# Kernel tuning notes

Hardware: AMD Instinct MI355X
Metric: run time of the kernel (lower is better)

Reference implementation:

```python
import jax, jax.numpy as jnp
import numpy as np

C = 2048  # per-input channels; concat channels = 2*C = 4096
B, H, W = 2, 64, 64


def setup_inputs() -> dict:
    key = jax.random.key(0)
    ks = jax.random.split(key, 8)
    s = 0.02
    return {
        "f_rgb": jax.random.normal(ks[0], (B, C, H, W), jnp.float32),
        "f_i": jax.random.normal(ks[1], (B, C, H, W), jnp.float32),
        "wq": jax.random.normal(ks[2], (C, 2 * C), jnp.float32) * s,
        "bq": jnp.zeros((C,), jnp.float32),
        "wk": jax.random.normal(ks[3], (C, 2 * C), jnp.float32) * s,
        "bk": jnp.zeros((C,), jnp.float32),
        "wv": jax.random.normal(ks[4], (2 * C, 2 * C), jnp.float32) * s,
        "bv": jnp.zeros((2 * C,), jnp.float32),
    }


def reference(f_rgb, f_i, wq, bq, wk, bk, wv, bv):
    b, c, h, w = f_rgb.shape
    n = h * w
    # concat along channels: [B, 2C, N]
    x = jnp.concatenate([f_rgb, f_i], axis=1).reshape(b, 2 * c, n)
    # 1x1 convs == per-pixel matmuls over channels
    Q = jnp.einsum('oc,bcn->bon', wq, x) + bq[None, :, None]  # [B, C, N]
    K = jnp.einsum('oc,bcn->bon', wk, x) + bk[None, :, None]  # [B, C, N]
    V = jnp.einsum('oc,bcn->bon', wv, x) + bv[None, :, None]  # [B, 2C, N]
    scale = jnp.sqrt(jnp.asarray(2 * c, jnp.float32))  # sqrt(channels of concat)
    attn = jax.nn.softmax(jnp.einsum('bcn,bcm->bnm', Q, K) / scale, axis=-1)  # [B, N, N]
    # out[b,c,n] = sum_m V[b,c,m] * attn[b,n,m]  (bmm(V, attn^T))
    out = jnp.einsum('bcm,bnm->bcn', V, attn).reshape(b, 2 * c, h, w)
    f_final = out[:, :c] + out[:, c:]
    return (f_final, f_rgb, f_i, attn)
```

## Files before the change

### kernel.cpp

```cpp
#include <hip/hip_runtime.h>
#include <hip/hip_bf16.h>


#define B_   2
#define C_   2048
#define N_   4096
#define C2_  4096

#define LDSB 131072

typedef __hip_bfloat16 bf16_t;
typedef __bf16 bf16x8 __attribute__((ext_vector_type(8)));
typedef float floatx4 __attribute__((ext_vector_type(4)));

__device__ inline void load_lds16(const void* g, void* l) {
  __builtin_amdgcn_global_load_lds(
      (const __attribute__((address_space(1))) void*)g,
      (__attribute__((address_space(3))) void*)l, 16, 0, 0);
}

__device__ inline unsigned short f2bf(float f) {
  return __builtin_bit_cast(unsigned short, __float2bfloat16(f));
}

__device__ inline void cstore(float* p, float v)  { *p = v; }
__device__ inline void cstore(bf16_t* p, float v) { *p = __float2bfloat16(v); }

template <typename OutT>
__global__ __launch_bounds__(512, 2) void gemm_bt8(
    const bf16_t* __restrict__ A, const bf16_t* __restrict__ Bt,
    OutT* __restrict__ Cm, int K, int lda, int ldb, int ldc,
    long long abst, long long bbst, long long cbst,
    const float* __restrict__ bias_m, const float* __restrict__ bias_n,
    float scale)
{
  extern __shared__ char smem[];

  const int tid  = threadIdx.x;
  const int lane = tid & 63;
  const int wave = tid >> 6;
  const int wm   = wave >> 2;
  const int wn   = wave & 3;
  const int fr   = lane & 15;
  const int kc   = lane >> 4;

  const long long bM = (long long)blockIdx.y * 256;
  const long long bN = (long long)blockIdx.x * 256;

  const bf16_t* Ab = A  + (long long)blockIdx.z * abst;
  const bf16_t* Bb = Bt + (long long)blockIdx.z * bbst;
  OutT*         Cb = Cm + (long long)blockIdx.z * cbst;

  const int srow = lane >> 3;
  const int scol = 8 * ((lane & 7) ^ srow);
  const bf16_t* gA = Ab + (bM + wave * 8 + srow) * (long long)lda + scol;
  const bf16_t* gB = Bb + (bN + wave * 8 + srow) * (long long)ldb + scol;
  char* sbase = smem + wave * 1024;

  auto stage = [&](int p, int ab, int h, int kt) {
    const long long ld = ab ? ldb : lda;
    const bf16_t* g = (ab ? gB : gA) + (long long)h * 128 * ld
                                     + (long long)kt * 64;
    char* l = sbase + p * 65536 + ab * 32768 + h * 16384;
    load_lds16(g,            l);
    load_lds16(g + 64 * ld,  l + 8192);
  };

  floatx4 acc[8][4];
#pragma unroll
  for (int i = 0; i < 8; i++)
#pragma unroll
    for (int j = 0; j < 4; j++) acc[i][j] = (floatx4){0.f, 0.f, 0.f, 0.f};

  bf16x8 af[4][2];
  bf16x8 bfr[4][2];

  auto readAh = [&](int p, int mh) {
#pragma unroll
    for (int i = 0; i < 4; i++) {
      const int row = (mh * 4 + i) * 32 + wm * 16 + fr;
      const char* rb = smem + p * 65536 + row * 128;
#pragma unroll
      for (int ks = 0; ks < 2; ks++)
        af[i][ks] = *(const bf16x8*)(rb +
            (((ks * 64) + kc * 16) ^ ((fr & 7) << 4)));
    }
  };
  auto readBh = [&](int p, int nh) {
#pragma unroll
    for (int j = 0; j < 2; j++) {
      const int row = (nh * 2 + j) * 64 + wn * 16 + fr;
      const char* rb = smem + p * 65536 + 32768 + row * 128;
#pragma unroll
      for (int ks = 0; ks < 2; ks++)
        bfr[nh * 2 + j][ks] = *(const bf16x8*)(rb +
            (((ks * 64) + kc * 16) ^ ((fr & 7) << 4)));
    }
  };
  auto quad = [&](int mh, int nh) {
    __builtin_amdgcn_s_setprio(1);
#pragma unroll
    for (int i = 0; i < 4; i++)
#pragma unroll
      for (int j = 0; j < 2; j++)
#pragma unroll
        for (int ks = 0; ks < 2; ks++)
          acc[mh * 4 + i][nh * 2 + j] = __builtin_amdgcn_mfma_f32_16x16x32_bf16(
              af[i][ks], bfr[nh * 2 + j][ks], acc[mh * 4 + i][nh * 2 + j],
              0, 0, 0);
    __builtin_amdgcn_s_setprio(0);
  };

  const int NT = K >> 6;

  {
    const int t1 = (NT > 1) ? 1 : 0;
    stage(0, 0, 0, 0); stage(0, 1, 0, 0);
    stage(0, 0, 1, 0); stage(0, 1, 1, 0);
    stage(1, 0, 0, t1); stage(1, 1, 0, t1);
  }
  asm volatile("s_waitcnt vmcnt(4)" ::: "memory");
  __builtin_amdgcn_s_barrier();

  for (int t = 0; t < NT; ++t) {
    const int p  = t & 1, q = p ^ 1;
    const int t1 = (t + 1 < NT) ? t + 1 : NT - 1;
    const int t2 = (t + 2 < NT) ? t + 2 : NT - 1;

    readAh(p, 0); readBh(p, 0);
    stage(q, 0, 1, t1);
    __builtin_amdgcn_s_barrier();
    quad(0, 0);
    __builtin_amdgcn_s_barrier();

    readBh(p, 1);
    stage(q, 1, 1, t1);
    __builtin_amdgcn_s_barrier();
    quad(0, 1);
    __builtin_amdgcn_s_barrier();

    readAh(p, 1);
    stage(p, 0, 0, t2);
    __builtin_amdgcn_s_barrier();
    quad(1, 1);
    __builtin_amdgcn_s_barrier();

    stage(p, 1, 0, t2);
    __builtin_amdgcn_s_barrier();
    quad(1, 0);
    asm volatile("s_waitcnt vmcnt(4)" ::: "memory");
    __builtin_amdgcn_s_barrier();
  }

  const int rown = (lane >> 4) * 4;
#pragma unroll
  for (int mi = 0; mi < 8; mi++) {
#pragma unroll
    for (int ni = 0; ni < 4; ni++) {
      const long long n = bN + ni * 64 + wn * 16 + fr;
      const float bnv = bias_n ? bias_n[n] : 0.f;
#pragma unroll
      for (int r = 0; r < 4; r++) {
        const long long m = bM + mi * 32 + wm * 16 + rown + r;
        const float bmv = bias_m ? bias_m[m] : 0.f;
        cstore(&Cb[m * (long long)ldc + n], acc[mi][ni][r] * scale + bnv + bmv);
      }
    }
  }
}

__global__ __launch_bounds__(256) void pack_xt(
    const float* __restrict__ f_rgb, const float* __restrict__ f_i,
    float* __restrict__ out_rgb, float* __restrict__ out_i,
    bf16_t* __restrict__ xt)
{
  const int b  = blockIdx.z >> 1;
  const int wh = blockIdx.z & 1;
  const float* src = (wh ? f_i : f_rgb) + (long long)b * C_ * N_;
  float*       pt  = (wh ? out_i : out_rgb) + (long long)b * C_ * N_;
  const int c0 = blockIdx.y * 64, n0 = blockIdx.x * 64;
  __shared__ float tile[64][65];

  const int tid = threadIdx.x;
  {
    const int tn = tid & 63, tc4 = tid >> 6;
#pragma unroll
    for (int r = 0; r < 16; r++) {
      const int c = tc4 * 16 + r;
      const long long idx = (long long)(c0 + c) * N_ + n0 + tn;
      const float v = src[idx];
      pt[idx] = v;
      tile[tn][c] = v;
    }
  }
  __syncthreads();
  {
    const int tc = tid & 63, tn4 = tid >> 6;
#pragma unroll
    for (int r = 0; r < 16; r++) {
      const int n = tn4 * 16 + r;
      xt[((long long)b * N_ + n0 + n) * C2_ + wh * C_ + c0 + tc] =
          __float2bfloat16(tile[n][tc]);
    }
  }
}

__global__ __launch_bounds__(256) void conv_wqk(
    const float* __restrict__ wq, const float* __restrict__ wk,
    unsigned short* __restrict__ dst)
{
  const long long i = ((long long)blockIdx.x * 256 + threadIdx.x) * 4;
  const int o = (int)(i >> 12);
  const long long c = i & 4095;
  const float* src = (o < C_) ? (wq + (long long)o * C2_ + c)
                              : (wk + (long long)(o - C_) * C2_ + c);
  const float4 f = *(const float4*)src;
  *(ushort4*)(dst + i) = make_ushort4(f2bf(f.x), f2bf(f.y), f2bf(f.z), f2bf(f.w));
}

__global__ __launch_bounds__(256) void conv_wvsum(
    const float* __restrict__ wv, unsigned short* __restrict__ dst)
{
  const long long i = ((long long)blockIdx.x * 256 + threadIdx.x) * 4;
  const float4 a = *(const float4*)(wv + i);
  const float4 b = *(const float4*)(wv + i + (long long)C_ * C2_);
  *(ushort4*)(dst + i) = make_ushort4(f2bf(a.x + b.x), f2bf(a.y + b.y),
                                      f2bf(a.z + b.z), f2bf(a.w + b.w));
}

__global__ __launch_bounds__(256) void conv_bias(
    const float* __restrict__ bq, const float* __restrict__ bk,
    const float* __restrict__ bv, float* __restrict__ bqk,
    float* __restrict__ bvsum)
{
  const int i = blockIdx.x * 256 + threadIdx.x;
  bqk[i] = (i < C_) ? bq[i] : bk[i - C_];
  if (i < C_) bvsum[i] = bv[i] + bv[i + C_];
}

__global__ __launch_bounds__(256) void softmax_rows(
    float* __restrict__ attn, bf16_t* __restrict__ attn_bf)
{
  const long long row = blockIdx.x;
  float*  p  = attn    + row * N_;
  bf16_t* pb = attn_bf + row * N_;
  const int tid = threadIdx.x;
  const int lane = tid & 63, wave = tid >> 6;

  float v[16];
  float mx = -3.4e38f;
#pragma unroll
  for (int i = 0; i < 16; i++) { v[i] = p[tid + i * 256]; mx = fmaxf(mx, v[i]); }
#pragma unroll
  for (int off = 32; off >= 1; off >>= 1) mx = fmaxf(mx, __shfl_xor(mx, off, 64));

  __shared__ float redm[4];
  __shared__ float reds[4];
  if (lane == 0) redm[wave] = mx;
  __syncthreads();
  mx = fmaxf(fmaxf(redm[0], redm[1]), fmaxf(redm[2], redm[3]));

  float s = 0.f;
#pragma unroll
  for (int i = 0; i < 16; i++) { v[i] = __expf(v[i] - mx); s += v[i]; }
#pragma unroll
  for (int off = 32; off >= 1; off >>= 1) s += __shfl_xor(s, off, 64);
  if (lane == 0) reds[wave] = s;
  __syncthreads();
  s = reds[0] + reds[1] + reds[2] + reds[3];
  const float inv = 1.f / s;
#pragma unroll
  for (int i = 0; i < 16; i++) {
    const float a = v[i] * inv;
    p[tid + i * 256]  = a;
    pb[tid + i * 256] = __float2bfloat16(a);
  }
}

extern "C" void kernel_launch(void* const* d_in, const int* in_sizes, int n_in,
                              void* d_out, int out_size, void* d_ws, size_t ws_size,
                              hipStream_t stream) {
  const float* f_rgb = (const float*)d_in[0];
  const float* f_i   = (const float*)d_in[1];
  const float* wq    = (const float*)d_in[2];
  const float* bq    = (const float*)d_in[3];
  const float* wk    = (const float*)d_in[4];
  const float* bk    = (const float*)d_in[5];
  const float* wv    = (const float*)d_in[6];
  const float* bv    = (const float*)d_in[7];

  float* out       = (float*)d_out;
  float* out_ff    = out;
  float* out_rgb   = out + (size_t)B_ * C_ * N_;
  float* out_fi    = out_rgb + (size_t)B_ * C_ * N_;
  float* out_attn  = out_fi + (size_t)B_ * C_ * N_;

  char* ws = (char*)d_ws;
  size_t off = 0;
  auto alloc = [&](size_t bytes) {
    size_t o = off; off += (bytes + 255) & ~(size_t)255; return o;
  };
  bf16_t* xt   = (bf16_t*)(ws + alloc((size_t)B_ * N_ * C2_ * 2));
  bf16_t* wqk  = (bf16_t*)(ws + alloc((size_t)C2_ * C2_ * 2));
  bf16_t* wvs  = (bf16_t*)(ws + alloc((size_t)C_ * C2_ * 2));
  bf16_t* qkt  = (bf16_t*)(ws + alloc((size_t)B_ * N_ * C2_ * 2));
  bf16_t* vsum = (bf16_t*)(ws + alloc((size_t)B_ * C_ * N_ * 2));
  bf16_t* abf  = (bf16_t*)(ws + alloc((size_t)B_ * N_ * N_ * 2));
  float*  bqk  = (float*)(ws + alloc((size_t)C2_ * 4));
  float*  bvs  = (float*)(ws + alloc((size_t)C_ * 4));
  (void)ws_size; (void)in_sizes; (void)n_in; (void)out_size;

  static bool attr_done = false;
  if (!attr_done) {
    (void)hipFuncSetAttribute((const void*)&gemm_bt8<bf16_t>,
        hipFuncAttributeMaxDynamicSharedMemorySize, LDSB);
    (void)hipFuncSetAttribute((const void*)&gemm_bt8<float>,
        hipFuncAttributeMaxDynamicSharedMemorySize, LDSB);
    attr_done = true;
  }

  const dim3 blk(256);
  const dim3 blk8(512);

  pack_xt<<<dim3(N_ / 64, C_ / 64, B_ * 2), blk, 0, stream>>>(
      f_rgb, f_i, out_rgb, out_fi, xt);
  conv_wqk<<<dim3((C2_ * C2_) / (4 * 256)), blk, 0, stream>>>(
      wq, wk, (unsigned short*)wqk);
  conv_wvsum<<<dim3((C_ * C2_) / (4 * 256)), blk, 0, stream>>>(
      wv, (unsigned short*)wvs);
  conv_bias<<<dim3(C2_ / 256), blk, 0, stream>>>(bq, bk, bv, bqk, bvs);

  const long long sNN = (long long)N_ * C2_;
  const long long sCN = (long long)C_ * N_;

  gemm_bt8<bf16_t><<<dim3(C2_ / 256, N_ / 256, B_), blk8, LDSB, stream>>>(
      xt, wqk, qkt, C2_, C2_, C2_, C2_, sNN, 0, sNN, nullptr, bqk, 1.0f);

  gemm_bt8<bf16_t><<<dim3(N_ / 256, C_ / 256, B_), blk8, LDSB, stream>>>(
      wvs, xt, vsum, C2_, C2_, C2_, N_, 0, sNN, sCN, bvs, nullptr, 1.0f);

  gemm_bt8<float><<<dim3(N_ / 256, N_ / 256, B_), blk8, LDSB, stream>>>(
      qkt, qkt + C_, out_attn, C_, C2_, C2_, N_, sNN, sNN, sNN,
      nullptr, nullptr, 1.0f / 64.0f);

  softmax_rows<<<dim3(B_ * N_), blk, 0, stream>>>(out_attn, abf);

  gemm_bt8<float><<<dim3(N_ / 256, C_ / 256, B_), blk8, LDSB, stream>>>(
      vsum, abf, out_ff, N_, N_, N_, N_, sCN, sNN, sCN,
      nullptr, nullptr, 1.0f);
}
```

Baseline: 1.131 ms.

## Swizzle GEMM workgroup order, deepen LDS prefetch, reorder MFMA loop, vectorize softmax

The GEMM kernel remaps linear workgroup IDs round-robin across eight groups, likely to spread consecutive tiles across the XCDs for better L2 locality. It also issues one more half-tile load ahead in the prologue and shifts the staging schedule so the global-to-LDS prefetch runs deeper, with the vmcnt wait raised to match. The MFMA loop is reordered so the k-step is outermost. Separately, the softmax kernel now uses float4 and ushort4 vector loads and stores in place of scalar accesses. The remapping assumes the workgroup count is divisible by eight, and the new staging order must keep buffer reuse hazards correct.

```diff
diff --git a/kernel.cpp b/kernel.cpp
--- a/kernel.cpp
+++ b/kernel.cpp
@@ -44,12 +44,22 @@
   const int fr   = lane & 15;
   const int kc   = lane >> 4;
 
-  const long long bM = (long long)blockIdx.y * 256;
-  const long long bN = (long long)blockIdx.x * 256;
-
-  const bf16_t* Ab = A  + (long long)blockIdx.z * abst;
-  const bf16_t* Bb = Bt + (long long)blockIdx.z * bbst;
-  OutT*         Cb = Cm + (long long)blockIdx.z * cbst;
+  const int gx  = gridDim.x, gy = gridDim.y;
+  const int nxy = gx * gy;
+  const int nwg = nxy * gridDim.z;
+  int wg = blockIdx.x + gx * (blockIdx.y + gy * blockIdx.z);
+  wg = (wg & 7) * (nwg >> 3) + (wg >> 3);
+  const int bz  = wg / nxy;
+  const int rxy = wg - bz * nxy;
+  const int by  = rxy / gx;
+  const int bx  = rxy - by * gx;
+
+  const long long bM = (long long)by * 256;
+  const long long bN = (long long)bx * 256;
+
+  const bf16_t* Ab = A  + (long long)bz * abst;
+  const bf16_t* Bb = Bt + (long long)bz * bbst;
+  OutT*         Cb = Cm + (long long)bz * cbst;
 
   const int srow = lane >> 3;
   const int scol = 8 * ((lane & 7) ^ srow);
@@ -100,11 +110,11 @@
   auto quad = [&](int mh, int nh) {
     __builtin_amdgcn_s_setprio(1);
 #pragma unroll
-    for (int i = 0; i < 4; i++)
-#pragma unroll
-      for (int j = 0; j < 2; j++)
-#pragma unroll
-        for (int ks = 0; ks < 2; ks++)
+    for (int ks = 0; ks < 2; ks++)
+#pragma unroll
+      for (int i = 0; i < 4; i++)
+#pragma unroll
+        for (int j = 0; j < 2; j++)
           acc[mh * 4 + i][nh * 2 + j] = __builtin_amdgcn_mfma_f32_16x16x32_bf16(
               af[i][ks], bfr[nh * 2 + j][ks], acc[mh * 4 + i][nh * 2 + j],
               0, 0, 0);
@@ -118,8 +128,9 @@
     stage(0, 0, 0, 0); stage(0, 1, 0, 0);
     stage(0, 0, 1, 0); stage(0, 1, 1, 0);
     stage(1, 0, 0, t1); stage(1, 1, 0, t1);
-  }
-  asm volatile("s_waitcnt vmcnt(4)" ::: "memory");
+    stage(1, 0, 1, t1);
+  }
+  asm volatile("s_waitcnt vmcnt(6)" ::: "memory");
   __builtin_amdgcn_s_barrier();
 
   for (int t = 0; t < NT; ++t) {
@@ -128,27 +139,27 @@
     const int t2 = (t + 2 < NT) ? t + 2 : NT - 1;
 
     readAh(p, 0); readBh(p, 0);
-    stage(q, 0, 1, t1);
+    stage(q, 1, 1, t1);
     __builtin_amdgcn_s_barrier();
     quad(0, 0);
     __builtin_amdgcn_s_barrier();
 
     readBh(p, 1);
-    stage(q, 1, 1, t1);
+    stage(p, 0, 0, t2);
     __builtin_amdgcn_s_barrier();
     quad(0, 1);
     __builtin_amdgcn_s_barrier();
 
     readAh(p, 1);
-    stage(p, 0, 0, t2);
+    stage(p, 1, 0, t2);
     __builtin_amdgcn_s_barrier();
     quad(1, 1);
     __builtin_amdgcn_s_barrier();
 
-    stage(p, 1, 0, t2);
+    stage(p, 0, 1, t2);
     __builtin_amdgcn_s_barrier();
     quad(1, 0);
-    asm volatile("s_waitcnt vmcnt(4)" ::: "memory");
+    asm volatile("s_waitcnt vmcnt(6)" ::: "memory");
     __builtin_amdgcn_s_barrier();
   }
 
@@ -242,15 +253,18 @@
     float* __restrict__ attn, bf16_t* __restrict__ attn_bf)
 {
   const long long row = blockIdx.x;
-  float*  p  = attn    + row * N_;
-  bf16_t* pb = attn_bf + row * N_;
+  float4*  p4  = (float4*)(attn + row * N_);
+  ushort4* pb4 = (ushort4*)(attn_bf + row * N_);
   const int tid = threadIdx.x;
   const int lane = tid & 63, wave = tid >> 6;
 
-  float v[16];
+  float4 v[4];
   float mx = -3.4e38f;
 #pragma unroll
-  for (int i = 0; i < 16; i++) { v[i] = p[tid + i * 256]; mx = fmaxf(mx, v[i]); }
+  for (int i = 0; i < 4; i++) {
+    v[i] = p4[tid + i * 256];
+    mx = fmaxf(mx, fmaxf(fmaxf(v[i].x, v[i].y), fmaxf(v[i].z, v[i].w)));
+  }
 #pragma unroll
   for (int off = 32; off >= 1; off >>= 1) mx = fmaxf(mx, __shfl_xor(mx, off, 64));
 
@@ -262,7 +276,11 @@
 
   float s = 0.f;
 #pragma unroll
-  for (int i = 0; i < 16; i++) { v[i] = __expf(v[i] - mx); s += v[i]; }
+  for (int i = 0; i < 4; i++) {
+    v[i].x = __expf(v[i].x - mx); v[i].y = __expf(v[i].y - mx);
+    v[i].z = __expf(v[i].z - mx); v[i].w = __expf(v[i].w - mx);
+    s += (v[i].x + v[i].y) + (v[i].z + v[i].w);
+  }
 #pragma unroll
   for (int off = 32; off >= 1; off >>= 1) s += __shfl_xor(s, off, 64);
   if (lane == 0) reds[wave] = s;
@@ -270,10 +288,12 @@
   s = reds[0] + reds[1] + reds[2] + reds[3];
   const float inv = 1.f / s;
 #pragma unroll
-  for (int i = 0; i < 16; i++) {
-    const float a = v[i] * inv;
-    p[tid + i * 256]  = a;
-    pb[tid + i * 256] = __float2bfloat16(a);
+  for (int i = 0; i < 4; i++) {
+    float4 a;
+    a.x = v[i].x * inv; a.y = v[i].y * inv;
+    a.z = v[i].z * inv; a.w = v[i].w * inv;
+    p4[tid + i * 256]  = a;
+    pb4[tid + i * 256] = make_ushort4(f2bf(a.x), f2bf(a.y), f2bf(a.z), f2bf(a.w));
   }
 }
 
```

Result: no change. 1.147 ms (+1.4%).
